# Kernel optimization log

Measured on AMD Instinct MI355X. Metric: run time of the kernel, lower is better.

Reference implementation:

```python
import jax, jax.numpy as jnp
import numpy as np


def setup_inputs() -> dict:
    key = jax.random.key(0)
    k1, k2 = jax.random.split(key)
    B, D, K = 8192, 4096, 16
    x = jax.random.normal(k1, (B, D), dtype=jnp.float32)
    # kaiming_uniform_(a=sqrt(5)) on [K, D]: bound = sqrt(6/((1+5)*fan_in)) = 1/sqrt(D)
    bound = 1.0 / np.sqrt(D)
    w = jax.random.uniform(k2, (K, D), dtype=jnp.float32, minval=-bound, maxval=bound)
    return {"x": x, "w": w}


def reference(x, w):
    # z[b,d] = x[b,d] * (1 + sum_{i=1..k} w[i-1,d] * x[b,(d+i) mod D])
    k = w.shape[0]
    acc = jnp.ones_like(x)
    for i in range(1, k + 1):
        acc = acc + w[i - 1][None, :] * jnp.roll(x, -i, axis=1)
    return x * acc
```

## Files before the change

kernel.cpp:

```cpp
#include <hip/hip_runtime.h>


#define D 4096
#define K 16
#define TPB 256
#define ROWS 16

__global__ __launch_bounds__(TPB) void quad_enhancer_kernel(
    const float* __restrict__ x, const float* __restrict__ w,
    float* __restrict__ out, int B) {
  const int dq = blockIdx.x * TPB + threadIdx.x;
  const int b0 = blockIdx.y * ROWS;

  float4 wv[K];
#pragma unroll
  for (int i = 0; i < K; ++i) {
    wv[i] = ((const float4*)(w + i * D))[dq];
  }

#pragma unroll 1
  for (int r = 0; r < ROWS; ++r) {
    const int b = b0 + r;
    if (b >= B) break;
    const float4* xrow = (const float4*)(x + (size_t)b * D);

    float xs[20];
#pragma unroll
    for (int j = 0; j < 5; ++j) {
      float4 v = xrow[(dq + j) & (D / 4 - 1)];
      xs[4 * j + 0] = v.x;
      xs[4 * j + 1] = v.y;
      xs[4 * j + 2] = v.z;
      xs[4 * j + 3] = v.w;
    }

    float ax = 1.0f, ay = 1.0f, az = 1.0f, aw = 1.0f;
#pragma unroll
    for (int i = 0; i < K; ++i) {
      ax = fmaf(wv[i].x, xs[0 + i + 1], ax);
      ay = fmaf(wv[i].y, xs[1 + i + 1], ay);
      az = fmaf(wv[i].z, xs[2 + i + 1], az);
      aw = fmaf(wv[i].w, xs[3 + i + 1], aw);
    }

    float4 o;
    o.x = xs[0] * ax;
    o.y = xs[1] * ay;
    o.z = xs[2] * az;
    o.w = xs[3] * aw;
    ((float4*)(out + (size_t)b * D))[dq] = o;
  }
}

extern "C" void kernel_launch(void* const* d_in, const int* in_sizes, int n_in,
                              void* d_out, int out_size, void* d_ws, size_t ws_size,
                              hipStream_t stream) {
  const float* x = (const float*)d_in[0];
  const float* w = (const float*)d_in[1];
  float* out = (float*)d_out;
  const int B = in_sizes[0] / D;

  dim3 grid(D / 4 / TPB, (B + ROWS - 1) / ROWS);
  quad_enhancer_kernel<<<grid, TPB, 0, stream>>>(x, w, out, B);
}
```

Baseline: 282.7 us.

## Stage x row tiles in LDS via direct global-to-LDS loads

Each block now loads an 8-row tile of x into shared memory with the global_load_lds builtin, plus a small halo, then reads the shifted windows from LDS instead of issuing five overlapping global float4 loads per row. Rows per block go from 16 to 8, with launch bounds asking for 4 blocks per CU. The aim is fewer redundant global/L2 accesses and more memory-level parallelism, at the cost of LDS usage, a block-wide barrier, and dropping the tail guard for B not divisible by 8.

```diff
diff --git a/kernel.cpp b/kernel.cpp
--- a/kernel.cpp
+++ b/kernel.cpp
@@ -2,53 +2,72 @@
 
 
 #define D 4096
+#define DG 1024
 #define K 16
 #define TPB 256
-#define ROWS 16
+#define TILE_B 8
+#define ROW_F4 260
+#define ROW_F (ROW_F4 * 4)
 
-__global__ __launch_bounds__(TPB) void quad_enhancer_kernel(
+__global__ __launch_bounds__(TPB, 4) void quad_enhancer_kernel(
     const float* __restrict__ x, const float* __restrict__ w,
-    float* __restrict__ out, int B) {
-  const int dq = blockIdx.x * TPB + threadIdx.x;
-  const int b0 = blockIdx.y * ROWS;
+    float* __restrict__ out) {
+  __shared__ float lds[TILE_B * ROW_F];
 
+  const int tid = threadIdx.x;
+  const int cg0 = blockIdx.x * TPB;
+  const int cg = cg0 + tid;
+  const int b0 = blockIdx.y * TILE_B;
+
+  const float4* w4 = (const float4*)w;
   float4 wv[K];
 #pragma unroll
-  for (int i = 0; i < K; ++i) {
-    wv[i] = ((const float4*)(w + i * D))[dq];
+  for (int i = 0; i < K; ++i) wv[i] = w4[i * DG + cg];
+
+  const float4* x4 = (const float4*)x;
+
+#pragma unroll
+  for (int r = 0; r < TILE_B; ++r) {
+    const float4* gptr = &x4[(size_t)(b0 + r) * DG + cg];
+    float* lptr = &lds[r * ROW_F + tid * 4];
+    __builtin_amdgcn_global_load_lds(
+        (const __attribute__((address_space(1))) void*)gptr,
+        (__attribute__((address_space(3))) void*)lptr, 16, 0, 0);
   }
+  if (tid < TILE_B * 4) {
+    const int r = tid >> 2, j = tid & 3;
+    float4 h = x4[(size_t)(b0 + r) * DG + ((cg0 + 256 + j) & (DG - 1))];
+    *(float4*)&lds[r * ROW_F + (256 + j) * 4] = h;
+  }
+  __syncthreads();
 
-#pragma unroll 1
-  for (int r = 0; r < ROWS; ++r) {
-    const int b = b0 + r;
-    if (b >= B) break;
-    const float4* xrow = (const float4*)(x + (size_t)b * D);
-
+  float4* out4 = (float4*)out;
+#pragma unroll 2
+  for (int r = 0; r < TILE_B; ++r) {
+    const float4* lrow = (const float4*)&lds[r * ROW_F];
     float xs[20];
 #pragma unroll
     for (int j = 0; j < 5; ++j) {
-      float4 v = xrow[(dq + j) & (D / 4 - 1)];
+      float4 v = lrow[tid + j];
       xs[4 * j + 0] = v.x;
       xs[4 * j + 1] = v.y;
       xs[4 * j + 2] = v.z;
       xs[4 * j + 3] = v.w;
     }
-
     float ax = 1.0f, ay = 1.0f, az = 1.0f, aw = 1.0f;
 #pragma unroll
     for (int i = 0; i < K; ++i) {
-      ax = fmaf(wv[i].x, xs[0 + i + 1], ax);
-      ay = fmaf(wv[i].y, xs[1 + i + 1], ay);
-      az = fmaf(wv[i].z, xs[2 + i + 1], az);
-      aw = fmaf(wv[i].w, xs[3 + i + 1], aw);
+      ax = fmaf(wv[i].x, xs[i + 1], ax);
+      ay = fmaf(wv[i].y, xs[i + 2], ay);
+      az = fmaf(wv[i].z, xs[i + 3], az);
+      aw = fmaf(wv[i].w, xs[i + 4], aw);
     }
-
     float4 o;
     o.x = xs[0] * ax;
     o.y = xs[1] * ay;
     o.z = xs[2] * az;
     o.w = xs[3] * aw;
-    ((float4*)(out + (size_t)b * D))[dq] = o;
+    out4[(size_t)(b0 + r) * DG + cg] = o;
   }
 }
 
@@ -60,6 +79,6 @@
   float* out = (float*)d_out;
   const int B = in_sizes[0] / D;
 
-  dim3 grid(D / 4 / TPB, (B + ROWS - 1) / ROWS);
-  quad_enhancer_kernel<<<grid, TPB, 0, stream>>>(x, w, out, B);
+  dim3 grid(DG / TPB, B / TILE_B);
+  quad_enhancer_kernel<<<grid, TPB, 0, stream>>>(x, w, out);
 }
```

Result: slower. 500.8 us (+77.2%).
